# Optimization experiments

Hardware: AMD Instinct MI355X
Metric: run time of the kernel (lower is better)

## Reference

```python
import jax, jax.numpy as jnp
import numpy as np

H, F, K, R = 8, 64, 10, 256  # num_heads, in_features, num_sines, num_realizations
B, L = 4, 2048


def setup_inputs() -> dict:
    key = jax.random.key(0)
    k1, k2, k3, k4, k5, k6 = jax.random.split(key, 6)
    return {
        "queries": jax.random.normal(k1, (B, L, H, F), dtype=jnp.float32),
        "keys": jax.random.normal(k2, (B, L, H, F), dtype=jnp.float32),
        "z": jax.random.normal(k3, (B, H, F, 2 * K, R), dtype=jnp.float32),
        "freqs": jax.random.normal(k4, (H, F, K), dtype=jnp.float32),
        "offsets": jax.random.normal(k5, (H, F, K), dtype=jnp.float32),
        "gains": jax.random.normal(k6, (H, F, K), dtype=jnp.float32),
    }


def reference(queries, keys, z, freqs, offsets, gains):
    h, f_dim, k_sines = freqs.shape
    length = queries.shape[1]
    r = z.shape[-1]
    # split positional / non-positional features (rest is empty here: key_dim == in_features)
    q_pos, q_rest = queries[..., :f_dim], queries[..., f_dim:]
    k_pos, k_rest = keys[..., :f_dim], keys[..., f_dim:]

    idx = jnp.arange(length, dtype=queries.dtype)  # linspace(0, L-1, L)
    fr = jax.nn.sigmoid(freqs)[:, :, None, :] / 2.0          # [H, F, 1, K]
    base = 2.0 * jnp.pi * fr * idx[None, None, :, None]       # [H, F, L, K]
    ph_q = base + offsets[:, :, None, :]
    ph_k = base
    # stack(cos, sin) on last axis then flatten -> interleaved cos0,sin0,... : [H, F, L, 2K]
    omega_q = jnp.stack([jnp.cos(ph_q), jnp.sin(ph_q)], axis=-1).reshape(h, f_dim, length, 2 * k_sines)
    omega_k = jnp.stack([jnp.cos(ph_k), jnp.sin(ph_k)], axis=-1).reshape(h, f_dim, length, 2 * k_sines)

    g = jnp.tile(jax.nn.softplus(gains), (1, 1, 2))           # [H, F, 2K] (block-repeated, as in torch .repeat)
    zs = z * g[None, :, :, :, None] / np.sqrt(r * f_dim).astype(np.float32)  # [B, H, F, 2K, R]

    # fused double contraction over f (in_features) and s (2K sines); equals
    # (omega @ z) permuted then multiplied by queries and summed over in_features
    qhat = jnp.einsum('hfls,bhfsr,blhf->blhr', omega_q, zs, q_pos)  # [B, L, H, R]
    khat = jnp.einsum('hfls,bhfsr,blhf->blhr', omega_k, zs, k_pos)

    qhat = jnp.concatenate([qhat, q_rest], axis=-1)
    khat = jnp.concatenate([khat, k_rest], axis=-1)
    return qhat, khat
```

## Files before the change

### kernel.cpp

```cpp
#include <hip/hip_runtime.h>
#include <math.h>


#define NH 8
#define NF 64
#define NK 10
#define NR 256
#define NB 4
#define NL 2048
#define KTOT 1280
#define BK 32
#define NCH (KTOT/BK)
#define NFRAG_B 16
#define WS_BPACK ((size_t)NB*NH*NCH*NFRAG_B*1024)
#define WS_TRIG  ((size_t)NH*NCH*2048*16*4)
#define WS_NEED2 (WS_BPACK + WS_TRIG)

typedef __attribute__((ext_vector_type(8))) short short8;
typedef __attribute__((ext_vector_type(4))) float f32x4;
typedef __attribute__((ext_vector_type(4))) unsigned int u32x4;
typedef __attribute__((ext_vector_type(2))) unsigned int u32x2;

static __device__ __forceinline__ unsigned short f2b(float f) {
    unsigned x = __float_as_uint(f);
    return (unsigned short)((x + 0x7FFFu + ((x >> 16) & 1u)) >> 16);
}
static __device__ __forceinline__ unsigned int pk2(float a, float b) {
    return (unsigned int)f2b(a) | ((unsigned int)f2b(b) << 16);
}
static __device__ __forceinline__ unsigned int cvtpk(float lo, float hi) {
    unsigned int r;
    asm("v_cvt_pk_bf16_f32 %0, %1, %2" : "=v"(r) : "v"(lo), "v"(hi));
    return r;
}
static __device__ __forceinline__ void gload_lds16(const void* g, void* l) {
    __builtin_amdgcn_global_load_lds(
        (const __attribute__((address_space(1))) unsigned int*)g,
        (__attribute__((address_space(3))) unsigned int*)l, 16, 0, 0);
}

__global__ __launch_bounds__(256)
void spe_prep(const float* __restrict__ z, const float* __restrict__ gains,
              unsigned char* __restrict__ bpack)
{
    __shared__ float s_g[NF*NK];
    const int ch  = blockIdx.x;
    const int bh  = blockIdx.y;
    const int h   = bh & 7;
    const int tid = threadIdx.x;
    for (int i = tid; i < NF*NK; i += 256)
        s_g[i] = log1pf(expf(gains[h*NF*NK + i])) * 0.0078125f;
    __syncthreads();
    const float* zb = z + (size_t)bh * KTOT * NR;
    unsigned char* dst = bpack + ((size_t)(bh*NCH + ch) * NFRAG_B) * 1024;
    #pragma unroll
    for (int it = 0; it < 4; ++it) {
        const int s  = tid + 256*it;
        const int fi = s >> 6;
        const int l  = s & 63;
        const int r  = fi*16 + (l & 15);
        const int k0 = ch*BK + (l >> 4)*8;
        u32x4 wv;
        #pragma unroll
        for (int jp = 0; jp < 4; ++jp) {
            const int ka = k0 + 2*jp, kb = ka + 1;
            const int fa = (ka*3277) >> 16; int sa = ka - fa*20; if (sa >= NK) sa -= NK;
            const int fb = (kb*3277) >> 16; int sb = kb - fb*20; if (sb >= NK) sb -= NK;
            const float va = zb[(size_t)ka*NR + r] * s_g[fa*NK + sa];
            const float vb = zb[(size_t)kb*NR + r] * s_g[fb*NK + sb];
            wv[jp] = pk2(va, vb);
        }
        *(u32x4*)(dst + (size_t)s*16) = wv;
    }
}

__global__ __launch_bounds__(256)
void spe_trig(const float* __restrict__ freqs, unsigned int* __restrict__ trig)
{
    const int t = blockIdx.x;
    const int h = blockIdx.y;
    const int tid = threadIdx.x;
    #pragma unroll
    for (int it = 0; it < 32; ++it) {
        const int site = tid + 256*it;
        const int l  = site >> 2;
        const int jg = site & 3;
        u32x4 wv;
        #pragma unroll
        for (int j = 0; j < 4; ++j) {
            const int kidx2 = t*16 + jg*4 + j;
            const float fv = freqs[h*640 + kidx2];
            const float fr = 0.5f / (1.0f + expf(-fv));
            const float x  = __builtin_amdgcn_fractf(fr * (float)l);
            wv[j] = pk2(__builtin_amdgcn_cosf(x), __builtin_amdgcn_sinf(x));
        }
        *(u32x4*)(trig + ((size_t)(h*NCH + t)*2048 + l)*16 + jg*4) = wv;
    }
}

#define OFF4_A   0
#define OFF4_POS 16384
#define OFF4_CS  32768
#define SMEM4_SZ 37888

__global__ __launch_bounds__(512, 4)
void spe_main4(const float* __restrict__ queries, const float* __restrict__ keys,
               const float* __restrict__ offsets,
               const unsigned char* __restrict__ bpack,
               const unsigned int* __restrict__ trig,
               float* __restrict__ out)
{
    __shared__ __attribute__((aligned(16))) unsigned char smem[SMEM4_SZ];
    const int tid  = threadIdx.x;
    const int lane = tid & 63;
    const int w    = tid >> 6;

    const int fb = blockIdx.x;
    const int h  = fb & 7;
    const int b  = (fb >> 3) & 3;
    const int l0 = (fb >> 5) * 64;
    const int bh = b*NH + h;

    float2* ld_cs = (float2*)(smem + OFF4_CS);
    unsigned short* pos_t = (unsigned short*)(smem + OFF4_POS);

    for (int i = tid; i < NF*NK; i += 512) {
        const float xo = __builtin_amdgcn_fractf(offsets[h*640 + i] * 0.15915494309189535f);
        ld_cs[i] = make_float2(__builtin_amdgcn_cosf(xo), __builtin_amdgcn_sinf(xo));
    }
    {
        const int r  = tid >> 2;
        const int f0 = (tid & 3) * 16;
        const int rl = r & 63;
        const float* src = (r < 64)
            ? queries + ((size_t)((b*NL + l0 + rl)*NH + h))*NF + f0
            : keys    + ((size_t)((b*NL + l0 + rl)*NH + h))*NF + f0;
        unsigned short* pdst = pos_t + ((r >> 6) << 12);
        #pragma unroll
        for (int j = 0; j < 4; ++j) {
            const float4 v = *(const float4*)(src + j*4);
            const int f = f0 + j*4;
            pdst[(f+0)*64 + rl] = f2b(v.x);
            pdst[(f+1)*64 + rl] = f2b(v.y);
            pdst[(f+2)*64 + rl] = f2b(v.z);
            pdst[(f+3)*64 + rl] = f2b(v.w);
        }
    }

    const unsigned char* bp = bpack + (size_t)bh * ((size_t)NCH*NFRAG_B*1024);
    const unsigned int*  tp = trig  + (size_t)h  * ((size_t)NCH*2048*16);

    const int wq   = w >> 2;
    const int wn   = w & 3;
    const size_t tstep = (size_t)2048*16;
    const unsigned int* tbase = tp + (size_t)(l0 + lane)*16 + wn*4;
    const int a_w  = ((wq*4 + (lane >> 4)) << 10) + ((wn*16 + (lane & 15)) << 4);
    const unsigned char* bwv = bp + (wn*4 << 10) + lane*16;

    u32x4 trEven = *(const u32x4*)(tbase);
    short8 bfEven[4], bfOdd[4];
    #pragma unroll
    for (int ni = 0; ni < 4; ++ni)
        bfEven[ni] = *(const short8*)(bwv + (ni << 10));
    u32x4 trOdd = *(const u32x4*)(tbase + tstep);
    __syncthreads();

    f32x4 acc[4][4];
    #pragma unroll
    for (int mi = 0; mi < 4; ++mi)
        #pragma unroll
        for (int ni = 0; ni < 4; ++ni)
            acc[mi][ni] = (f32x4){0.f, 0.f, 0.f, 0.f};

    auto synthA = [&](int t, const u32x4 tr) -> u32x4 {
        u32x4 av_;
        const int kb = t*16 + wn*4;
        #pragma unroll
        for (int p = 0; p < 4; ++p) {
            const int kidx = kb + p;
            const int f    = (kidx * 6554) >> 16;
            const float ck = __uint_as_float(tr[p] << 16);
            const float sk = __uint_as_float(tr[p] & 0xffff0000u);
            const float pv = __uint_as_float(((unsigned)pos_t[wq*4096 + f*64 + lane]) << 16);
            float c, s;
            if (wq == 0) {
                const float2 cs = ld_cs[kidx];
                c = ck*cs.x - sk*cs.y;
                s = sk*cs.x + ck*cs.y;
            } else { c = ck; s = sk; }
            av_[p] = cvtpk(c*pv, s*pv);
        }
        return av_;
    };

    u32x4 av = synthA(0, trEven);

    auto iter = [&](int t, int par, short8 (&bfC)[4], short8 (&bfN)[4],
                    const u32x4 trUse, u32x4& trLoad) {
        *(u32x4*)(smem + OFF4_A + par*8192 + a_w) = av;
        asm volatile("s_waitcnt lgkmcnt(0)" ::: "memory");
        __builtin_amdgcn_sched_barrier(0);
        __builtin_amdgcn_s_barrier();

        if (t + 1 < NCH) {
            const unsigned char* bn = bwv + (size_t)(t+1)*16384;
            #pragma unroll
            for (int ni = 0; ni < 4; ++ni)
                bfN[ni] = *(const short8*)(bn + (ni << 10));
        }
        if (t + 2 < NCH)
            trLoad = *(const u32x4*)(tbase + (size_t)(t+2)*tstep);

        if (t + 1 < NCH) av = synthA(t + 1, trUse);

        #pragma unroll
        for (int mi = 0; mi < 4; ++mi) {
            const short8 af = *(const short8*)(smem + OFF4_A + par*8192
                                               + ((wq*4 + mi) << 10) + (lane << 4));
            #pragma unroll
            for (int ni = 0; ni < 4; ++ni)
                acc[mi][ni] = __builtin_amdgcn_mfma_f32_16x16x32_bf16(af, bfC[ni], acc[mi][ni], 0, 0, 0);
        }
    };

    #pragma unroll 1
    for (int t = 0; t < NCH; t += 2) {
        iter(t,     0, bfEven, bfOdd,  trOdd,  trEven);
        iter(t + 1, 1, bfOdd,  bfEven, trEven, trOdd);
    }

    const size_t qk_off = (size_t)wq * ((size_t)NB*NL*NH*NR);
    const int row_l = (lane >> 4) * 4;
    const int col_r = lane & 15;
    #pragma unroll
    for (int mi = 0; mi < 4; ++mi) {
        const int lg = l0 + mi*16 + row_l;
        #pragma unroll
        for (int ni = 0; ni < 4; ++ni) {
            const int rg = wn*64 + ni*16 + col_r;
            const f32x4 v = acc[mi][ni];
            #pragma unroll
            for (int q = 0; q < 4; ++q)
                out[qk_off + ((size_t)((b*NL + lg + q)*NH + h))*NR + rg] = v[q];
        }
    }
}

#define OFF_B   0
#define OFF_A   49152
#define OFF_POS 57344
#define OFF_FR  73728
#define OFF_CO  76288
#define OFF_SO  78848
#define SMEM_SZ 81408

__global__ __launch_bounds__(512, 4)
void spe_main(const float* __restrict__ queries, const float* __restrict__ keys,
              const float* __restrict__ freqs, const float* __restrict__ offsets,
              const unsigned char* __restrict__ bpack, float* __restrict__ out)
{
    __shared__ __attribute__((aligned(16))) unsigned char smem[SMEM_SZ];
    const int tid  = threadIdx.x;
    const int lane = tid & 63;
    const int w    = tid >> 6;
    const int l0   = blockIdx.x * 64;
    const int bh   = blockIdx.y;
    const int b = bh >> 3, h = bh & 7;

    float* ld_fr = (float*)(smem + OFF_FR);
    float* ld_co = (float*)(smem + OFF_CO);
    float* ld_so = (float*)(smem + OFF_SO);
    unsigned short* pos_t = (unsigned short*)(smem + OFF_POS);

    for (int i = tid; i < NF*NK; i += 512) {
        const float fv = freqs[h*NF*NK + i];
        ld_fr[i] = 0.5f / (1.0f + expf(-fv));
        const float xo = __builtin_amdgcn_fractf(offsets[h*NF*NK + i] * 0.15915494309189535f);
        ld_co[i] = __builtin_amdgcn_cosf(xo);
        ld_so[i] = __builtin_amdgcn_sinf(xo);
    }
    {
        const int r  = tid >> 2;
        const int f0 = (tid & 3) * 16;
        const int rl = r & 63;
        const float* src = (r < 64)
            ? queries + ((size_t)((b*NL + l0 + rl)*NH + h))*NF + f0
            : keys    + ((size_t)((b*NL + l0 + rl)*NH + h))*NF + f0;
        unsigned short* pdst = pos_t + ((r >> 6) << 12);
        #pragma unroll
        for (int j = 0; j < 4; ++j) {
            const float4 v = *(const float4*)(src + j*4);
            const int f = f0 + j*4;
            pdst[(f+0)*64 + rl] = f2b(v.x);
            pdst[(f+1)*64 + rl] = f2b(v.y);
            pdst[(f+2)*64 + rl] = f2b(v.z);
            pdst[(f+3)*64 + rl] = f2b(v.w);
        }
    }
    __syncthreads();

    const unsigned char* bp = bpack + (size_t)bh * ((size_t)NCH*NFRAG_B*1024);
    const int fi0 = w*2;
    gload_lds16(bp + (size_t)fi0*1024 + lane*16,               smem + OFF_B + (fi0  <<10));
    gload_lds16(bp + (size_t)(fi0+1)*1024 + lane*16,           smem + OFF_B + ((fi0+1)<<10));
    gload_lds16(bp + (size_t)(NFRAG_B + fi0)*1024 + lane*16,   smem + OFF_B + 16384 + (fi0  <<10));
    gload_lds16(bp + (size_t)(NFRAG_B + fi0+1)*1024 + lane*16, smem + OFF_B + 16384 + ((fi0+1)<<10));

    const int wm = w >> 2, wn = w & 3;
    f32x4 acc[4][4];
    #pragma unroll
    for (int mi = 0; mi < 4; ++mi)
        #pragma unroll
        for (int ni = 0; ni < 4; ++ni)
            acc[mi][ni] = (f32x4){0.f, 0.f, 0.f, 0.f};

    const int rq   = ((w & 1) << 5) | (lane & 31);
    const int oct  = w >> 1;
    const int half = lane >> 5;
    const float lf = (float)(l0 + rq);
    const unsigned short* posq = pos_t;
    const unsigned short* posk = pos_t + 4096;
    const int aw_q = OFF_A + ((rq >> 4) << 10) + ((oct*16 + (rq & 15)) << 4) + (half << 3);
    const int aw_k = aw_q + 4096;

    auto synthA = [&](int t, u32x2& q01, u32x2& k01) {
        #pragma unroll
        for (int p = 0; p < 2; ++p) {
            const int kk   = t*BK + oct*8 + half*4 + p*2;
            const int f    = (kk*3277) >> 16;
            const int srem = kk - f*20;
            const int kidx = f*NK + (srem >> 1);
            const float x  = __builtin_amdgcn_fractf(ld_fr[kidx] * lf);
            const float ck = __builtin_amdgcn_cosf(x);
            const float sk = __builtin_amdgcn_sinf(x);
            const float co = ld_co[kidx], so = ld_so[kidx];
            const float cq = ck*co - sk*so;
            const float sq = sk*co + ck*so;
            const float pq = __uint_as_float(((unsigned)posq[f*64 + rq]) << 16);
            const float pk = __uint_as_float(((unsigned)posk[f*64 + rq]) << 16);
            q01[p] = cvtpk(cq*pq, sq*pq);
            k01[p] = cvtpk(ck*pk, sk*pk);
        }
    };

    u32x2 q01, k01;
    synthA(0, q01, k01);

    int bsel  = 0;
    int bsel2 = 2;
    for (int t = 0; t < NCH; ++t) {
        if (t < NCH-1) { asm volatile("s_waitcnt vmcnt(2)" ::: "memory"); }
        else           { asm volatile("s_waitcnt vmcnt(0)" ::: "memory"); }
        __builtin_amdgcn_sched_barrier(0);
        __builtin_amdgcn_s_barrier();

        if (t + 2 < NCH) {
            unsigned char* Bn = smem + OFF_B + bsel2*16384;
            gload_lds16(bp + (size_t)((t+2)*NFRAG_B + fi0)*1024 + lane*16,
                        Bn + (fi0<<10));
            gload_lds16(bp + (size_t)((t+2)*NFRAG_B + fi0+1)*1024 + lane*16,
                        Bn + ((fi0+1)<<10));
        }

        *(u32x2*)(smem + aw_q) = q01;
        *(u32x2*)(smem + aw_k) = k01;
        asm volatile("s_waitcnt lgkmcnt(0)" ::: "memory");
        __builtin_amdgcn_sched_barrier(0);
        __builtin_amdgcn_s_barrier();

        const unsigned char* Bc = smem + OFF_B + bsel*16384;
        short8 bf[4];
        #pragma unroll
        for (int ni = 0; ni < 4; ++ni)
            bf[ni] = *(const short8*)(Bc + ((wn*4 + ni) << 10) + (lane << 4));

        if (t + 1 < NCH) synthA(t + 1, q01, k01);

        #pragma unroll
        for (int mi = 0; mi < 4; ++mi) {
            const short8 af = *(const short8*)(smem + OFF_A + ((wm*4 + mi) << 10) + (lane << 4));
            #pragma unroll
            for (int ni = 0; ni < 4; ++ni)
                acc[mi][ni] = __builtin_amdgcn_mfma_f32_16x16x32_bf16(af, bf[ni], acc[mi][ni], 0, 0, 0);
        }

        bsel  = (bsel  == 2) ? 0 : bsel  + 1;
        bsel2 = (bsel2 == 2) ? 0 : bsel2 + 1;
    }

    const size_t qk_off = (size_t)wm * ((size_t)NB*NL*NH*NR);
    const int row_l = (lane >> 4) * 4;
    const int col_r = lane & 15;
    #pragma unroll
    for (int mi = 0; mi < 4; ++mi) {
        const int lg = l0 + mi*16 + row_l;
        #pragma unroll
        for (int ni = 0; ni < 4; ++ni) {
            const int rg = wn*64 + ni*16 + col_r;
            const f32x4 v = acc[mi][ni];
            #pragma unroll
            for (int q = 0; q < 4; ++q)
                out[qk_off + ((size_t)((b*NL + lg + q)*NH + h))*NR + rg] = v[q];
        }
    }
}

extern "C" void kernel_launch(void* const* d_in, const int* in_sizes, int n_in,
                              void* d_out, int out_size, void* d_ws, size_t ws_size,
                              hipStream_t stream) {
    const float* queries = (const float*)d_in[0];
    const float* keys    = (const float*)d_in[1];
    const float* z       = (const float*)d_in[2];
    const float* freqs   = (const float*)d_in[3];
    const float* offsets = (const float*)d_in[4];
    const float* gains   = (const float*)d_in[5];
    float* out = (float*)d_out;

    unsigned char* bpack = (unsigned char*)d_ws;
    spe_prep<<<dim3(NCH, NB*NH), 256, 0, stream>>>(z, gains, bpack);

    if (ws_size >= WS_NEED2) {
        unsigned int* trig = (unsigned int*)(bpack + WS_BPACK);
        spe_trig<<<dim3(NCH, NH), 256, 0, stream>>>(freqs, trig);
        spe_main4<<<dim3(1024), 512, 0, stream>>>(queries, keys, offsets, bpack, trig, out);
    } else {
        spe_main<<<dim3(NL/64, NB*NH), 512, 0, stream>>>(queries, keys, freqs, offsets, bpack, out);
    }
}
```

Before: 148.8 us.

## Switch main GEMM to 32x32x16 MFMA with repacked B and trig layouts

Replaces the 16x16x32 bf16 MFMA tiles in the main kernel with 32x32x16 tiles, and repacks the z fragments and the trig table to match the new operand layout. Each wave now covers a 64x64 output block as 2x2 tiles across two k-steps. This cuts the number of MFMA issues and operand reads per useful FLOP. It also wraps the MFMA block in s_setprio, at the cost of a more complex output scatter pattern and a separate prep kernel for the fallback path.

Result: slower. 275.4 us (+85.1%).

```diff
diff --git a/kernel.cpp b/kernel.cpp
--- a/kernel.cpp
+++ b/kernel.cpp
@@ -13,11 +13,12 @@
 #define NCH (KTOT/BK)
 #define NFRAG_B 16
 #define WS_BPACK ((size_t)NB*NH*NCH*NFRAG_B*1024)
-#define WS_TRIG  ((size_t)NH*NCH*2048*16*4)
+#define WS_TRIG  ((size_t)NH*NCH*4*2048*16)
 #define WS_NEED2 (WS_BPACK + WS_TRIG)
 
 typedef __attribute__((ext_vector_type(8))) short short8;
 typedef __attribute__((ext_vector_type(4))) float f32x4;
+typedef __attribute__((ext_vector_type(16))) float f32x16;
 typedef __attribute__((ext_vector_type(4))) unsigned int u32x4;
 typedef __attribute__((ext_vector_type(2))) unsigned int u32x2;
 
@@ -40,8 +41,8 @@
 }
 
 __global__ __launch_bounds__(256)
-void spe_prep(const float* __restrict__ z, const float* __restrict__ gains,
-              unsigned char* __restrict__ bpack)
+void spe_prep32(const float* __restrict__ z, const float* __restrict__ gains,
+                unsigned char* __restrict__ bpack)
 {
     __shared__ float s_g[NF*NK];
     const int ch  = blockIdx.x;
@@ -55,11 +56,13 @@
     unsigned char* dst = bpack + ((size_t)(bh*NCH + ch) * NFRAG_B) * 1024;
     #pragma unroll
     for (int it = 0; it < 4; ++it) {
-        const int s  = tid + 256*it;
-        const int fi = s >> 6;
-        const int l  = s & 63;
-        const int r  = fi*16 + (l & 15);
-        const int k0 = ch*BK + (l >> 4)*8;
+        const int s   = tid + 256*it;
+        const int fid = s >> 6;
+        const int l   = s & 63;
+        const int ks  = fid >> 3;
+        const int ct  = fid & 7;
+        const int r   = ct*32 + (l & 31);
+        const int k0  = ch*BK + ks*16 + (l >> 5)*8;
         u32x4 wv;
         #pragma unroll
         for (int jp = 0; jp < 4; ++jp) {
@@ -75,6 +78,41 @@
 }
 
 __global__ __launch_bounds__(256)
+void spe_prep16(const float* __restrict__ z, const float* __restrict__ gains,
+                unsigned char* __restrict__ bpack)
+{
+    __shared__ float s_g[NF*NK];
+    const int ch  = blockIdx.x;
+    const int bh  = blockIdx.y;
+    const int h   = bh & 7;
+    const int tid = threadIdx.x;
+    for (int i = tid; i < NF*NK; i += 256)
+        s_g[i] = log1pf(expf(gains[h*NF*NK + i])) * 0.0078125f;
+    __syncthreads();
+    const float* zb = z + (size_t)bh * KTOT * NR;
+    unsigned char* dst = bpack + ((size_t)(bh*NCH + ch) * NFRAG_B) * 1024;
+    #pragma unroll
+    for (int it = 0; it < 4; ++it) {
+        const int s  = tid + 256*it;
+        const int fi = s >> 6;
+        const int l  = s & 63;
+        const int r  = fi*16 + (l & 15);
+        const int k0 = ch*BK + (l >> 4)*8;
+        u32x4 wv;
+        #pragma unroll
+        for (int jp = 0; jp < 4; ++jp) {
+            const int ka = k0 + 2*jp, kb = ka + 1;
+            const int fa = (ka*3277) >> 16; int sa = ka - fa*20; if (sa >= NK) sa -= NK;
+            const int fb = (kb*3277) >> 16; int sb = kb - fb*20; if (sb >= NK) sb -= NK;
+            const float va = zb[(size_t)ka*NR + r] * s_g[fa*NK + sa];
+            const float vb = zb[(size_t)kb*NR + r] * s_g[fb*NK + sb];
+            wv[jp] = pk2(va, vb);
+        }
+        *(u32x4*)(dst + (size_t)s*16) = wv;
+    }
+}
+
+__global__ __launch_bounds__(256)
 void spe_trig(const float* __restrict__ freqs, unsigned int* __restrict__ trig)
 {
     const int t = blockIdx.x;
@@ -83,34 +121,34 @@
     #pragma unroll
     for (int it = 0; it < 32; ++it) {
         const int site = tid + 256*it;
-        const int l  = site >> 2;
-        const int jg = site & 3;
+        const int l = site & 2047;
+        const int g = site >> 11;
         u32x4 wv;
         #pragma unroll
         for (int j = 0; j < 4; ++j) {
-            const int kidx2 = t*16 + jg*4 + j;
-            const float fv = freqs[h*640 + kidx2];
+            const int kidx = t*16 + g*4 + j;
+            const float fv = freqs[h*640 + kidx];
             const float fr = 0.5f / (1.0f + expf(-fv));
             const float x  = __builtin_amdgcn_fractf(fr * (float)l);
             wv[j] = pk2(__builtin_amdgcn_cosf(x), __builtin_amdgcn_sinf(x));
         }
-        *(u32x4*)(trig + ((size_t)(h*NCH + t)*2048 + l)*16 + jg*4) = wv;
-    }
-}
-
-#define OFF4_A   0
-#define OFF4_POS 16384
-#define OFF4_CS  32768
-#define SMEM4_SZ 37888
+        *(u32x4*)(trig + ((size_t)((h*NCH + t)*4 + g)*2048 + l)*4) = wv;
+    }
+}
+
+#define OFF5_A   0
+#define OFF5_POS 16384
+#define OFF5_CS  32768
+#define SMEM5_SZ 37888
 
 __global__ __launch_bounds__(512, 4)
-void spe_main4(const float* __restrict__ queries, const float* __restrict__ keys,
+void spe_main5(const float* __restrict__ queries, const float* __restrict__ keys,
                const float* __restrict__ offsets,
                const unsigned char* __restrict__ bpack,
                const unsigned int* __restrict__ trig,
                float* __restrict__ out)
 {
-    __shared__ __attribute__((aligned(16))) unsigned char smem[SMEM4_SZ];
+    __shared__ __attribute__((aligned(16))) unsigned char smem[SMEM5_SZ];
     const int tid  = threadIdx.x;
     const int lane = tid & 63;
     const int w    = tid >> 6;
@@ -121,8 +159,8 @@
     const int l0 = (fb >> 5) * 64;
     const int bh = b*NH + h;
 
-    float2* ld_cs = (float2*)(smem + OFF4_CS);
-    unsigned short* pos_t = (unsigned short*)(smem + OFF4_POS);
+    float2* ld_cs = (float2*)(smem + OFF5_CS);
+    unsigned short* pos_t = (unsigned short*)(smem + OFF5_POS);
 
     for (int i = tid; i < NF*NK; i += 512) {
         const float xo = __builtin_amdgcn_fractf(offsets[h*640 + i] * 0.15915494309189535f);
@@ -148,42 +186,49 @@
     }
 
     const unsigned char* bp = bpack + (size_t)bh * ((size_t)NCH*NFRAG_B*1024);
-    const unsigned int*  tp = trig  + (size_t)h  * ((size_t)NCH*2048*16);
-
-    const int wq   = w >> 2;
-    const int wn   = w & 3;
-    const size_t tstep = (size_t)2048*16;
-    const unsigned int* tbase = tp + (size_t)(l0 + lane)*16 + wn*4;
-    const int a_w  = ((wq*4 + (lane >> 4)) << 10) + ((wn*16 + (lane & 15)) << 4);
-    const unsigned char* bwv = bp + (wn*4 << 10) + lane*16;
+
+    const int wq = w >> 2, wn = w & 3;
+    const int sqk  = w >> 2;
+    const int ks_s = (w >> 1) & 1;
+    const int rt_s = w & 1;
+    const int row_s = rt_s*32 + (lane & 31);
+    const int g_s   = ks_s*2 + (lane >> 5);
+    const int a_w   = ((sqk*4 + ks_s*2 + rt_s) << 10) + (lane << 4);
+    const unsigned int* tbase =
+        trig + ((size_t)(h*NCH)*4 + g_s)*2048*4 + (size_t)(l0 + row_s)*4;
+    const size_t tstep = (size_t)4*2048*4;
 
     u32x4 trEven = *(const u32x4*)(tbase);
     short8 bfEven[4], bfOdd[4];
     #pragma unroll
-    for (int ni = 0; ni < 4; ++ni)
-        bfEven[ni] = *(const short8*)(bwv + (ni << 10));
+    for (int fi = 0; fi < 4; ++fi) {
+        const int fid = (fi >> 1)*8 + wn*2 + (fi & 1);
+        bfEven[fi] = *(const short8*)(bp + (fid << 10) + lane*16);
+    }
     u32x4 trOdd = *(const u32x4*)(tbase + tstep);
     __syncthreads();
 
-    f32x4 acc[4][4];
-    #pragma unroll
-    for (int mi = 0; mi < 4; ++mi)
-        #pragma unroll
-        for (int ni = 0; ni < 4; ++ni)
-            acc[mi][ni] = (f32x4){0.f, 0.f, 0.f, 0.f};
+    f32x16 acc[2][2];
+    #pragma unroll
+    for (int mi = 0; mi < 2; ++mi)
+        #pragma unroll
+        for (int ni = 0; ni < 2; ++ni)
+            #pragma unroll
+            for (int q = 0; q < 16; ++q)
+                acc[mi][ni][q] = 0.0f;
 
     auto synthA = [&](int t, const u32x4 tr) -> u32x4 {
         u32x4 av_;
-        const int kb = t*16 + wn*4;
+        const int kb = t*16 + g_s*4;
         #pragma unroll
         for (int p = 0; p < 4; ++p) {
             const int kidx = kb + p;
             const int f    = (kidx * 6554) >> 16;
             const float ck = __uint_as_float(tr[p] << 16);
             const float sk = __uint_as_float(tr[p] & 0xffff0000u);
-            const float pv = __uint_as_float(((unsigned)pos_t[wq*4096 + f*64 + lane]) << 16);
+            const float pv = __uint_as_float(((unsigned)pos_t[sqk*4096 + f*64 + row_s]) << 16);
             float c, s;
-            if (wq == 0) {
+            if (sqk == 0) {
                 const float2 cs = ld_cs[kidx];
                 c = ck*cs.x - sk*cs.y;
                 s = sk*cs.x + ck*cs.y;
@@ -197,30 +242,42 @@
 
     auto iter = [&](int t, int par, short8 (&bfC)[4], short8 (&bfN)[4],
                     const u32x4 trUse, u32x4& trLoad) {
-        *(u32x4*)(smem + OFF4_A + par*8192 + a_w) = av;
+        *(u32x4*)(smem + OFF5_A + par*8192 + a_w) = av;
         asm volatile("s_waitcnt lgkmcnt(0)" ::: "memory");
         __builtin_amdgcn_sched_barrier(0);
         __builtin_amdgcn_s_barrier();
 
+        short8 af[2][2];
+        #pragma unroll
+        for (int ks = 0; ks < 2; ++ks)
+            #pragma unroll
+            for (int mi = 0; mi < 2; ++mi)
+                af[ks][mi] = *(const short8*)(smem + OFF5_A + par*8192
+                                              + ((wq*4 + ks*2 + mi) << 10) + (lane << 4));
+
         if (t + 1 < NCH) {
-            const unsigned char* bn = bwv + (size_t)(t+1)*16384;
-            #pragma unroll
-            for (int ni = 0; ni < 4; ++ni)
-                bfN[ni] = *(const short8*)(bn + (ni << 10));
+            const unsigned char* bn = bp + (size_t)(t+1)*16384;
+            #pragma unroll
+            for (int fi = 0; fi < 4; ++fi) {
+                const int fid = (fi >> 1)*8 + wn*2 + (fi & 1);
+                bfN[fi] = *(const short8*)(bn + (fid << 10) + lane*16);
+            }
         }
         if (t + 2 < NCH)
             trLoad = *(const u32x4*)(tbase + (size_t)(t+2)*tstep);
 
         if (t + 1 < NCH) av = synthA(t + 1, trUse);
 
-        #pragma unroll
-        for (int mi = 0; mi < 4; ++mi) {
-            const short8 af = *(const short8*)(smem + OFF4_A + par*8192
-                                               + ((wq*4 + mi) << 10) + (lane << 4));
-            #pragma unroll
-            for (int ni = 0; ni < 4; ++ni)
-                acc[mi][ni] = __builtin_amdgcn_mfma_f32_16x16x32_bf16(af, bfC[ni], acc[mi][ni], 0, 0, 0);
-        }
+        __builtin_amdgcn_s_setprio(1);
+        #pragma unroll
+        for (int ks = 0; ks < 2; ++ks)
+            #pragma unroll
+            for (int mi = 0; mi < 2; ++mi)
+                #pragma unroll
+                for (int ni = 0; ni < 2; ++ni)
+                    acc[mi][ni] = __builtin_amdgcn_mfma_f32_32x32x16_bf16(
+                        af[ks][mi], bfC[ks*2 + ni], acc[mi][ni], 0, 0, 0);
+        __builtin_amdgcn_s_setprio(0);
     };
 
     #pragma unroll 1
@@ -230,18 +287,18 @@
     }
 
     const size_t qk_off = (size_t)wq * ((size_t)NB*NL*NH*NR);
-    const int row_l = (lane >> 4) * 4;
-    const int col_r = lane & 15;
-    #pragma unroll
-    for (int mi = 0; mi < 4; ++mi) {
-        const int lg = l0 + mi*16 + row_l;
-        #pragma unroll
-        for (int ni = 0; ni < 4; ++ni) {
-            const int rg = wn*64 + ni*16 + col_r;
-            const f32x4 v = acc[mi][ni];
-            #pragma unroll
-            for (int q = 0; q < 4; ++q)
-                out[qk_off + ((size_t)((b*NL + lg + q)*NH + h))*NR + rg] = v[q];
+    const int col_b = wn*64 + (lane & 31);
+    const int row_b = 4*(lane >> 5);
+    #pragma unroll
+    for (int mi = 0; mi < 2; ++mi) {
+        #pragma unroll
+        for (int ni = 0; ni < 2; ++ni) {
+            const int rg = col_b + ni*32;
+            #pragma unroll
+            for (int q = 0; q < 16; ++q) {
+                const int lg = l0 + mi*32 + row_b + (q & 3) + 8*(q >> 2);
+                out[qk_off + ((size_t)((b*NL + lg)*NH + h))*NR + rg] = acc[mi][ni][q];
+            }
         }
     }
 }
@@ -417,13 +474,14 @@
     float* out = (float*)d_out;
 
     unsigned char* bpack = (unsigned char*)d_ws;
-    spe_prep<<<dim3(NCH, NB*NH), 256, 0, stream>>>(z, gains, bpack);
 
     if (ws_size >= WS_NEED2) {
         unsigned int* trig = (unsigned int*)(bpack + WS_BPACK);
+        spe_prep32<<<dim3(NCH, NB*NH), 256, 0, stream>>>(z, gains, bpack);
         spe_trig<<<dim3(NCH, NH), 256, 0, stream>>>(freqs, trig);
-        spe_main4<<<dim3(1024), 512, 0, stream>>>(queries, keys, offsets, bpack, trig, out);
+        spe_main5<<<dim3(1024), 512, 0, stream>>>(queries, keys, offsets, bpack, trig, out);
     } else {
+        spe_prep16<<<dim3(NCH, NB*NH), 256, 0, stream>>>(z, gains, bpack);
         spe_main<<<dim3(NL/64, NB*NH), 512, 0, stream>>>(queries, keys, freqs, offsets, bpack, out);
     }
 }
```
